# Kernel optimization log

Measured on AMD Instinct MI355X. Metric: run time of the kernel, lower is better.

The kernel has to match this reference:

```python
import jax, jax.numpy as jnp
import numpy as np
from jax import lax

STRIDES = (8, 16, 32)
REG_MAX = 16
NUM_CLASSES = 80
CLS_OUT = NUM_CLASSES + 1  # 81
REG_OUT = 4 * (REG_MAX + 1)  # 68
IN_CH = (128, 256, 512)
FEAT_HW = ((80, 80), (40, 40), (20, 20))
BATCH = 32


def _conv3(x, w, b):
    # x: [N,C,H,W], w: [O,C,3,3] -> SAME padding, stride 1
    y = lax.conv_general_dilated(x, w, (1, 1), 'SAME',
                                 dimension_numbers=('NCHW', 'OIHW', 'NCHW'))
    return y + b[None, :, None, None]


def _level_priors(h, w, stride):
    # matches get_single_level_center_priors: x fastest-varying
    xs = jnp.arange(w, dtype=jnp.float32) * stride
    ys = jnp.arange(h, dtype=jnp.float32) * stride
    x = jnp.tile(xs[None, :], (h, 1)).reshape(-1)
    y = jnp.tile(ys[:, None], (1, w)).reshape(-1)
    s = jnp.full((h * w,), float(stride), dtype=jnp.float32)
    return jnp.stack([x, y, s, s], axis=-1)  # [HW,4]


def setup_inputs() -> dict:
    key = jax.random.key(0)
    ks = jax.random.split(key, 16)
    d = {}
    for i, (c, (h, w)) in enumerate(zip(IN_CH, FEAT_HW)):
        d[f'x{i}'] = jax.random.normal(ks[i], (BATCH, c, h, w), dtype=jnp.float32)
    ki = 3
    for i, c in enumerate(IN_CH):
        d[f'wc{i}'] = jax.random.normal(ks[ki], (CLS_OUT, c, 3, 3), dtype=jnp.float32) * 0.02; ki += 1
        d[f'bc{i}'] = jnp.full((CLS_OUT,), -4.595, dtype=jnp.float32)  # bias_init_with_prob(0.01)
        d[f'wr{i}'] = jax.random.normal(ks[ki], (REG_OUT, c, 3, 3), dtype=jnp.float32) * 0.02; ki += 1
        d[f'br{i}'] = jnp.zeros((REG_OUT,), dtype=jnp.float32)
    d['scales'] = jnp.ones((3,), dtype=jnp.float32)
    return d


def reference(x0, x1, x2, wc0, bc0, wr0, br0, wc1, bc1, wr1, br1,
              wc2, bc2, wr2, br2, scales):
    xs = (x0, x1, x2)
    wcs, bcs = (wc0, wc1, wc2), (bc0, bc1, bc2)
    wrs, brs = (wr0, wr1, wr2), (br0, br1, br2)
    cls_list, box_list, prior_list = [], [], []
    for i in range(3):
        x = xs[i]
        N, _, H, W = x.shape
        # forward_single (stacked_convs=0 -> no tower convs)
        bbox = _conv3(x, wrs[i], brs[i]) * scales[i]          # [N,68,H,W]
        bbox = bbox.reshape(N, 4, REG_MAX + 1, H, W)
        bbox = jax.nn.softmax(bbox, axis=2)                   # softmax over bins
        bbox = bbox.reshape(N, 4, REG_MAX + 1, H * W).transpose(0, 3, 1, 2)  # [N,HW,4,17]
        cls = jax.nn.sigmoid(_conv3(x, wcs[i], bcs[i]))       # [N,81,H,W]
        cls = cls.reshape(N, CLS_OUT, H * W).transpose(0, 2, 1)  # [N,HW,81]
        cls_list.append(cls)
        box_list.append(bbox)
        prior_list.append(_level_priors(H, W, STRIDES[i]))
    cls_scores = jnp.concatenate(cls_list, axis=1)[:, :, :NUM_CLASSES]  # [N,A,80]
    bbox_dist = jnp.concatenate(box_list, axis=1)                        # [N,A,4,17]
    priors = jnp.concatenate(prior_list, axis=0)[None]                   # [1,A,4]
    # Integral: expectation over bins 0..reg_max
    project = jnp.arange(REG_MAX + 1, dtype=bbox_dist.dtype)
    dist = jnp.einsum('nafr,r->naf', bbox_dist, project)                 # [N,A,4]
    dist = dist * priors[..., 2, None]                                   # scale by stride
    # distance2bbox
    px, py = priors[..., 0], priors[..., 1]
    bboxes = jnp.stack([px - dist[..., 0], py - dist[..., 1],
                        px + dist[..., 2], py + dist[..., 3]], axis=-1)  # [N,A,4]
    return cls_scores, bboxes
```

## Files before the change

### kernel.cpp

```cpp
#include <hip/hip_runtime.h>
#include <hip/hip_bf16.h>
#include <math.h>

#define BATCH   32
#define A_TOTAL 8400
#define NCLS    80

typedef __attribute__((ext_vector_type(8))) short bf16x8;
typedef __attribute__((ext_vector_type(4))) float f32x4;

__device__ __forceinline__ short f2bf(float f) {
    union { float f; unsigned u; } v; v.f = f;
    unsigned u = v.u + 0x7fffu + ((v.u >> 16) & 1u);
    return (short)(u >> 16);
}

__device__ __forceinline__ void stage16(const void* g, void* ldsp) {
    __builtin_amdgcn_global_load_lds(
        (const __attribute__((address_space(1))) unsigned int*)g,
        (__attribute__((address_space(3))) unsigned int*)ldsp, 16, 0, 0);
}

template<int C>
__global__ __launch_bounds__(256) void prep_w(const float* __restrict__ wc,
                                              const float* __restrict__ wr,
                                              __hip_bfloat16* __restrict__ af) {
    const int KC = C / 32;
    const int total = 9 * KC * 10 * 64;
    int idx = blockIdx.x * 256 + threadIdx.x;
    if (idx >= total) return;
    int l   = idx & 63;
    int rem = idx >> 6;
    int mf  = rem % 10;
    int kc  = (rem / 10) % KC;
    int tap = rem / (10 * KC);
    int m     = mf * 16 + (l & 15);
    int cbase = kc * 32 + (l >> 4) * 8;
    short v[8];
#pragma unroll
    for (int j = 0; j < 8; ++j) {
        int c = cbase + j;
        float w = 0.f;
        if (m < 80)        w = wc[((size_t)m * C + c) * 9 + tap];
        else if (m < 148)  w = wr[((size_t)(m - 80) * C + c) * 9 + tap];
        v[j] = f2bf(w);
    }
    *(bf16x8*)((short*)af + (size_t)idx * 8) = *(bf16x8*)v;
}

template<int C, int H, int W>
__global__ __launch_bounds__(256) void transpose_x(const float* __restrict__ x,
                                                   __hip_bfloat16* __restrict__ xT) {
    const int CC  = C / 64;
    const int KC  = C / 32;
    const int PW  = W + 2;
    const int PHW = (H + 2) * PW;
    int b   = blockIdx.x;
    int cch = b % CC;
    int y   = (b / CC) % H;
    int n   = b / (CC * H);
    __shared__ float sm[64][W + 1];
    const float* src = x + (((size_t)n * C + cch * 64) * H + y) * W;
    for (int i = threadIdx.x; i < 64 * (W / 4); i += 256) {
        int c = i / (W / 4), f4 = i % (W / 4);
        float4 v = *(const float4*)(src + (size_t)c * H * W + f4 * 4);
        sm[c][f4 * 4 + 0] = v.x;
        sm[c][f4 * 4 + 1] = v.y;
        sm[c][f4 * 4 + 2] = v.z;
        sm[c][f4 * 4 + 3] = v.w;
    }
    __syncthreads();
    short* base = (short*)xT + (size_t)n * KC * 4 * PHW * 8;
    for (int u = threadIdx.x; u < W * 8; u += 256) {
        int g8 = u / W, xc = u % W;
        int kc = cch * 2 + (g8 >> 2);
        int j  = g8 & 3;
        short v[8];
#pragma unroll
        for (int jj = 0; jj < 8; ++jj) v[jj] = f2bf(sm[g8 * 8 + jj][xc]);
        *(bf16x8*)(base + (((size_t)(kc * 4 + j)) * PHW + (y + 1) * PW + xc + 1) * 8) =
            *(bf16x8*)v;
    }
    bf16x8 z = (bf16x8)(short)0;
    if (threadIdx.x < 16) {
        int g8 = threadIdx.x >> 1, side = threadIdx.x & 1;
        int kc = cch * 2 + (g8 >> 2), j = g8 & 3;
        *(bf16x8*)(base + (((size_t)(kc * 4 + j)) * PHW + (y + 1) * PW + side * (W + 1)) * 8) = z;
    }
    if (y == 0) {
        for (int u = threadIdx.x; u < PW * 8; u += 256) {
            int g8 = u / PW, col = u % PW;
            int kc = cch * 2 + (g8 >> 2), j = g8 & 3;
            *(bf16x8*)(base + (((size_t)(kc * 4 + j)) * PHW + col) * 8) = z;
        }
    }
    if (y == H - 1) {
        for (int u = threadIdx.x; u < PW * 8; u += 256) {
            int g8 = u / PW, col = u % PW;
            int kc = cch * 2 + (g8 >> 2), j = g8 & 3;
            *(bf16x8*)(base + (((size_t)(kc * 4 + j)) * PHW + (H + 1) * PW + col) * 8) = z;
        }
    }
}

template<int C, int H, int W, int STRIDE, int A_OFFp, int LVL, int NT, int KS, int NBLK>
__global__ __launch_bounds__(256, NBLK) void gemm_head(
    const __hip_bfloat16* __restrict__ xT,
    const __hip_bfloat16* __restrict__ af,
    const float* __restrict__ bc, const float* __restrict__ br,
    const float* __restrict__ scales,
    float* __restrict__ out_cls, float* __restrict__ out_box,
    float* __restrict__ pbuf) {
    constexpr int HW     = H * W;
    constexpr int PW     = W + 2;
    constexpr int PHW    = (H + 2) * PW;
    constexpr int NF     = NT / 32;
    constexpr int TILES  = (HW + NT - 1) / NT;
    constexpr int KC     = C / 32;
    constexpr int KCS    = KC / KS;
    constexpr int DYMAX  = (NT - 1) / W + 1;
    constexpr int NSTAGE = NT + 2 * DYMAX + 2 * W + 7;
    constexpr int NS16   = NSTAGE * 16;
    constexpr int NG     = NSTAGE * 4;
    constexpr int ITB    = (NG + 255) / 256;
    constexpr int BSZ    = ITB * 4096;
    constexpr int EPI    = 68 * (NT + 4) * 4;
    constexpr int LDSB   = (KS > 1) ? (2 * BSZ) : ((2 * BSZ) > EPI ? (2 * BSZ) : EPI);
    static_assert(ITB <= 9, "B staging spread exceeds tap steps");

    __shared__ __align__(16) char lds[LDSB];

    constexpr int NWG = BATCH * TILES * KS;
    const int bid  = blockIdx.x;
    const int swz  = (bid & 7) * (NWG / 8) + (bid >> 3);
    const int ks   = swz % KS;
    const int rest = swz / KS;
    const int tile = rest % TILES;
    const int n    = rest / TILES;

    const int tid   = threadIdx.x;
    const int l     = tid & 63;
    const int wid   = tid >> 6;
    const int mhalf = wid & 1;
    const int nhalf = wid >> 1;
    const int lr    = l & 15;
    const int kg    = l >> 4;

    const char* xb  = (const char*)xT + (size_t)n * KC * 4 * PHW * 16;
    const char* afc = (const char*)af;

    const int p0    = tile * NT;
    const int qbase = (p0 / W) * PW + (p0 % W);

    int blane[NF];
#pragma unroll
    for (int nf = 0; nf < NF; ++nf) {
        int p  = p0 + (nhalf * NF + nf) * 16 + lr;
        int qc = (p / W + 1) * PW + (p % W) + 1;
        blane[nf] = kg * NS16 + (qc - (W + 3) - qbase) * 16;
    }

    f32x4 acc[5][NF];
#pragma unroll
    for (int mf = 0; mf < 5; ++mf)
#pragma unroll
        for (int nf = 0; nf < NF; ++nf) acc[mf][nf] = (f32x4)0.f;

    auto stageB = [&](int it, int kc, unsigned dstbase) {
        int idx = it * 256 + tid;
        int j = idx / NSTAGE; if (j > 3) j = 3;
        int q = qbase + (idx - j * NSTAGE);
        if (q > PHW - 1) q = PHW - 1;
        stage16(xb + ((size_t)(kc * 4 + j) * PHW + q) * 16,
                &lds[dstbase + it * 4096 + wid * 1024]);
    };

    const int kc0 = ks * KCS;
#pragma unroll
    for (int it = 0; it < ITB; ++it) stageB(it, kc0, 0);
    __syncthreads();

    unsigned curB = 0;

#pragma unroll 1
    for (int kk = 0; kk < KCS; ++kk) {
        const int kc = kc0 + kk;
#pragma unroll
        for (int tap = 0; tap < 9; ++tap) {
            if (tap < ITB && kk + 1 < KCS)
                stageB(tap, kc + 1, curB ^ BSZ);
            const char* asrc = afc + (size_t)(tap * KC + kc) * 10240 +
                               mhalf * 5120 + l * 16;
            bf16x8 a[5];
#pragma unroll
            for (int mf = 0; mf < 5; ++mf)
                a[mf] = *(const bf16x8*)(asrc + mf * 1024);
            const int imm = ((tap / 3) * PW + (tap % 3)) * 16;
#pragma unroll
            for (int nf = 0; nf < NF; ++nf) {
                bf16x8 b = *(const bf16x8*)&lds[curB + blane[nf] + imm];
#pragma unroll
                for (int mf = 0; mf < 5; ++mf)
                    acc[mf][nf] = __builtin_amdgcn_mfma_f32_16x16x32_bf16(
                        a[mf], b, acc[mf][nf], 0, 0, 0);
            }
        }
        __syncthreads();
        curB ^= BSZ;
    }

    if constexpr (KS > 1) {
        float* pb = pbuf + (size_t)((n * TILES + tile) * KS + ks) * (160 * NT);
#pragma unroll
        for (int mf = 0; mf < 5; ++mf)
#pragma unroll
            for (int nf = 0; nf < NF; ++nf) {
                int col = (nhalf * NF + nf) * 16 + lr;
#pragma unroll
                for (int r = 0; r < 4; ++r) {
                    int ch = mhalf * 80 + mf * 16 + kg * 4 + r;
                    pb[ch * NT + col] = acc[mf][nf][r];
                }
            }
        return;
    } else {
        const float sc = scales[LVL];
        float* smf = (float*)lds;

        if (mhalf == 0) {
            float4 bias[5];
#pragma unroll
            for (int mf = 0; mf < 5; ++mf)
                bias[mf] = *(const float4*)(bc + mf * 16 + kg * 4);
#pragma unroll
            for (int nf = 0; nf < NF; ++nf) {
                int p = p0 + (nhalf * NF + nf) * 16 + lr;
                if (p < HW) {
                    float* oc = out_cls + ((size_t)n * A_TOTAL + A_OFFp + p) * NCLS;
#pragma unroll
                    for (int mf = 0; mf < 5; ++mf) {
                        f32x4 v = acc[mf][nf];
                        float4 s;
                        s.x = 1.f / (1.f + expf(-(v[0] + bias[mf].x)));
                        s.y = 1.f / (1.f + expf(-(v[1] + bias[mf].y)));
                        s.z = 1.f / (1.f + expf(-(v[2] + bias[mf].z)));
                        s.w = 1.f / (1.f + expf(-(v[3] + bias[mf].w)));
                        *(float4*)(oc + mf * 16 + kg * 4) = s;
                    }
                }
            }
        } else {
#pragma unroll
            for (int mf = 0; mf < 5; ++mf)
#pragma unroll
                for (int nf = 0; nf < NF; ++nf) {
                    int lpx = (nhalf * NF + nf) * 16 + lr;
#pragma unroll
                    for (int r = 0; r < 4; ++r) {
                        int ch = mf * 16 + kg * 4 + r;
                        if (ch < 68) smf[ch * (NT + 4) + lpx] = acc[mf][nf][r];
                    }
                }
        }
        __syncthreads();

#pragma unroll
        for (int uu = 0; uu < NT / 64; ++uu) {
            int u   = uu * 256 + tid;
            int f   = u >> 7;
            int lpx = u & 127;
            if (NT == 64) { f = (u >> 6) & 3; lpx = u & 63; }
            int p = p0 + lpx;
            if (f < 4 && p < HW) {
                float lg[17];
                float m = -1e30f;
#pragma unroll
                for (int r = 0; r < 17; ++r) {
                    lg[r] = (smf[(f * 17 + r) * (NT + 4) + lpx] + br[f * 17 + r]) * sc;
                    m = fmaxf(m, lg[r]);
                }
                float ssum = 0.f, esum = 0.f;
#pragma unroll
                for (int r = 0; r < 17; ++r) {
                    float e = expf(lg[r] - m);
                    ssum += e;
                    esum += e * (float)r;
                }
                const float dist = esum / ssum * (float)STRIDE;
                const int py = p / W, px = p % W;
                const float base = (f & 1) ? (float)(py * STRIDE) : (float)(px * STRIDE);
                const float val  = (f < 2) ? (base - dist) : (base + dist);
                out_box[((size_t)n * A_TOTAL + A_OFFp + p) * 4 + f] = val;
            }
        }
    }
}

template<int H, int W, int STRIDE, int A_OFFp, int LVL, int TILES, int KS>
__global__ __launch_bounds__(256) void reduce_epi(
    const float* __restrict__ pbuf,
    const float* __restrict__ bc, const float* __restrict__ br,
    const float* __restrict__ scales,
    float* __restrict__ out_cls, float* __restrict__ out_box) {
    constexpr int HW = H * W;
    const int bid  = blockIdx.x;
    const int tile = bid % TILES;
    const int n    = bid / TILES;
    const int tid  = threadIdx.x;
    const float* pb = pbuf + (size_t)(n * TILES + tile) * KS * 10240;

    __shared__ float smf[160 * 66];
    for (int idx = tid; idx < 160 * 64; idx += 256) {
        float s = 0.f;
#pragma unroll
        for (int k = 0; k < KS; ++k) s += pb[k * 10240 + idx];
        smf[(idx >> 6) * 66 + (idx & 63)] = s;
    }
    __syncthreads();

    const int q = tid >> 6;
    const int t = tid & 63;
    const int p = tile * 64 + t;
    if (p < HW) {
        float* oc = out_cls + ((size_t)n * A_TOTAL + A_OFFp + p) * NCLS + q * 20;
#pragma unroll
        for (int k = 0; k < 20; k += 4) {
            float4 v;
            v.x = 1.f / (1.f + expf(-(smf[(q * 20 + k + 0) * 66 + t] + bc[q * 20 + k + 0])));
            v.y = 1.f / (1.f + expf(-(smf[(q * 20 + k + 1) * 66 + t] + bc[q * 20 + k + 1])));
            v.z = 1.f / (1.f + expf(-(smf[(q * 20 + k + 2) * 66 + t] + bc[q * 20 + k + 2])));
            v.w = 1.f / (1.f + expf(-(smf[(q * 20 + k + 3) * 66 + t] + bc[q * 20 + k + 3])));
            *(float4*)(oc + k) = v;
        }
        const float sc = scales[LVL];
        float lg[17];
        float m = -1e30f;
#pragma unroll
        for (int r = 0; r < 17; ++r) {
            lg[r] = (smf[(80 + q * 17 + r) * 66 + t] + br[q * 17 + r]) * sc;
            m = fmaxf(m, lg[r]);
        }
        float ssum = 0.f, esum = 0.f;
#pragma unroll
        for (int r = 0; r < 17; ++r) {
            float e = expf(lg[r] - m);
            ssum += e;
            esum += e * (float)r;
        }
        const float dist = esum / ssum * (float)STRIDE;
        const int py = p / W, px = p % W;
        const float base = (q & 1) ? (float)(py * STRIDE) : (float)(px * STRIDE);
        const float val  = (q < 2) ? (base - dist) : (base + dist);
        out_box[((size_t)n * A_TOTAL + A_OFFp + p) * 4 + q] = val;
    }
}

extern "C" void kernel_launch(void* const* d_in, const int* in_sizes, int n_in,
                              void* d_out, int out_size, void* d_ws, size_t ws_size,
                              hipStream_t stream) {
    const float* x0  = (const float*)d_in[0];
    const float* x1  = (const float*)d_in[1];
    const float* x2  = (const float*)d_in[2];
    const float* wc0 = (const float*)d_in[3];
    const float* bc0 = (const float*)d_in[4];
    const float* wr0 = (const float*)d_in[5];
    const float* br0 = (const float*)d_in[6];
    const float* wc1 = (const float*)d_in[7];
    const float* bc1 = (const float*)d_in[8];
    const float* wr1 = (const float*)d_in[9];
    const float* br1 = (const float*)d_in[10];
    const float* wc2 = (const float*)d_in[11];
    const float* bc2 = (const float*)d_in[12];
    const float* wr2 = (const float*)d_in[13];
    const float* br2 = (const float*)d_in[14];
    const float* scl = (const float*)d_in[15];

    float* out_cls = (float*)d_out;
    float* out_box = (float*)d_out + (size_t)BATCH * A_TOTAL * NCLS;

    __hip_bfloat16* af  = (__hip_bfloat16*)d_ws;
    __hip_bfloat16* af0 = af;
    __hip_bfloat16* af1 = af + 184320;
    __hip_bfloat16* af2 = af + 552960;
    __hip_bfloat16* xT  = af + 1290240;
    float* pbuf = (float*)((char*)xT + 15859712);

    prep_w<128><<<dim3(90),  256, 0, stream>>>(wc0, wr0, af0);
    prep_w<256><<<dim3(180), 256, 0, stream>>>(wc1, wr1, af1);
    prep_w<512><<<dim3(360), 256, 0, stream>>>(wc2, wr2, af2);

    transpose_x<128, 80, 80><<<dim3(32 * 80 * 2), 256, 0, stream>>>(x0, xT);
    gemm_head<128, 80, 80, 8, 0, 0, 128, 1, 3><<<dim3(32 * 50), 256, 0, stream>>>(
        xT, af0, bc0, br0, scl, out_cls, out_box, nullptr);

    transpose_x<256, 40, 40><<<dim3(32 * 40 * 4), 256, 0, stream>>>(x1, xT);
    gemm_head<256, 40, 40, 16, 6400, 1, 64, 1, 4><<<dim3(32 * 25), 256, 0, stream>>>(
        xT, af1, bc1, br1, scl, out_cls, out_box, nullptr);

    transpose_x<512, 20, 20><<<dim3(32 * 20 * 8), 256, 0, stream>>>(x2, xT);
    gemm_head<512, 20, 20, 32, 8000, 2, 64, 4, 4><<<dim3(32 * 7 * 4), 256, 0, stream>>>(
        xT, af2, bc2, br2, scl, out_cls, out_box, pbuf);
    reduce_epi<20, 20, 32, 8000, 2, 7, 4><<<dim3(32 * 7), 256, 0, stream>>>(
        pbuf, bc2, br2, scl, out_cls, out_box);
}
```

Before: 281.2 us.

## Prefetch A fragments one tap ahead, use fast sigmoid/exp, retune level tiles

The GEMM inner loop now loads the weight (A) fragments for the next tap into a second register set while the current tap's MFMAs run, hiding global load latency. Sigmoid and softmax switch to __expf and hardware reciprocal, and the box epilogue loop is generalised to any tile width. The level-1 launch moves to 96-pixel tiles with fewer blocks, and the last template parameter changes for levels 1 and 2. The changes cost extra VGPRs and slightly lower-precision transcendentals, and the prefetch on the final step reads one A block past the end.

```diff
diff --git a/kernel.cpp b/kernel.cpp
--- a/kernel.cpp
+++ b/kernel.cpp
@@ -13,6 +13,10 @@
     union { float f; unsigned u; } v; v.f = f;
     unsigned u = v.u + 0x7fffu + ((v.u >> 16) & 1u);
     return (short)(u >> 16);
+}
+
+__device__ __forceinline__ float fsig(float x) {
+    return __builtin_amdgcn_rcpf(1.f + __expf(-x));
 }
 
 __device__ __forceinline__ void stage16(const void* g, void* ldsp) {
@@ -174,8 +178,18 @@
         stage16(xb + ((size_t)(kc * 4 + j) * PHW + q) * 16,
                 &lds[dstbase + it * 4096 + wid * 1024]);
     };
+    auto loadA = [&](bf16x8* dst, int step) {
+        const char* asrc = afc + (size_t)step * 10240 + mhalf * 5120 + l * 16;
+#pragma unroll
+        for (int mf = 0; mf < 5; ++mf)
+            dst[mf] = *(const bf16x8*)(asrc + mf * 1024);
+    };
 
     const int kc0 = ks * KCS;
+
+    bf16x8 acur[5], anxt[5];
+    loadA(acur, kc0);
+
 #pragma unroll
     for (int it = 0; it < ITB; ++it) stageB(it, kc0, 0);
     __syncthreads();
@@ -189,12 +203,8 @@
         for (int tap = 0; tap < 9; ++tap) {
             if (tap < ITB && kk + 1 < KCS)
                 stageB(tap, kc + 1, curB ^ BSZ);
-            const char* asrc = afc + (size_t)(tap * KC + kc) * 10240 +
-                               mhalf * 5120 + l * 16;
-            bf16x8 a[5];
-#pragma unroll
-            for (int mf = 0; mf < 5; ++mf)
-                a[mf] = *(const bf16x8*)(asrc + mf * 1024);
+            const int nstep = (tap == 8) ? (kc + 1) : ((tap + 1) * KC + kc);
+            loadA(anxt, nstep);
             const int imm = ((tap / 3) * PW + (tap % 3)) * 16;
 #pragma unroll
             for (int nf = 0; nf < NF; ++nf) {
@@ -202,8 +212,10 @@
 #pragma unroll
                 for (int mf = 0; mf < 5; ++mf)
                     acc[mf][nf] = __builtin_amdgcn_mfma_f32_16x16x32_bf16(
-                        a[mf], b, acc[mf][nf], 0, 0, 0);
+                        acur[mf], b, acc[mf][nf], 0, 0, 0);
             }
+#pragma unroll
+            for (int mf = 0; mf < 5; ++mf) acur[mf] = anxt[mf];
         }
         __syncthreads();
         curB ^= BSZ;
@@ -241,10 +253,10 @@
                     for (int mf = 0; mf < 5; ++mf) {
                         f32x4 v = acc[mf][nf];
                         float4 s;
-                        s.x = 1.f / (1.f + expf(-(v[0] + bias[mf].x)));
-                        s.y = 1.f / (1.f + expf(-(v[1] + bias[mf].y)));
-                        s.z = 1.f / (1.f + expf(-(v[2] + bias[mf].z)));
-                        s.w = 1.f / (1.f + expf(-(v[3] + bias[mf].w)));
+                        s.x = fsig(v[0] + bias[mf].x);
+                        s.y = fsig(v[1] + bias[mf].y);
+                        s.z = fsig(v[2] + bias[mf].z);
+                        s.w = fsig(v[3] + bias[mf].w);
                         *(float4*)(oc + mf * 16 + kg * 4) = s;
                     }
                 }
@@ -264,14 +276,11 @@
         }
         __syncthreads();
 
-#pragma unroll
-        for (int uu = 0; uu < NT / 64; ++uu) {
-            int u   = uu * 256 + tid;
-            int f   = u >> 7;
-            int lpx = u & 127;
-            if (NT == 64) { f = (u >> 6) & 3; lpx = u & 63; }
-            int p = p0 + lpx;
-            if (f < 4 && p < HW) {
+        for (int u = tid; u < 4 * NT; u += 256) {
+            int f   = u / NT;
+            int lpx = u % NT;
+            int p   = p0 + lpx;
+            if (p < HW) {
                 float lg[17];
                 float m = -1e30f;
 #pragma unroll
@@ -282,11 +291,11 @@
                 float ssum = 0.f, esum = 0.f;
 #pragma unroll
                 for (int r = 0; r < 17; ++r) {
-                    float e = expf(lg[r] - m);
+                    float e = __expf(lg[r] - m);
                     ssum += e;
                     esum += e * (float)r;
                 }
-                const float dist = esum / ssum * (float)STRIDE;
+                const float dist = esum * __builtin_amdgcn_rcpf(ssum) * (float)STRIDE;
                 const int py = p / W, px = p % W;
                 const float base = (f & 1) ? (float)(py * STRIDE) : (float)(px * STRIDE);
                 const float val  = (f < 2) ? (base - dist) : (base + dist);
@@ -326,10 +335,10 @@
 #pragma unroll
         for (int k = 0; k < 20; k += 4) {
             float4 v;
-            v.x = 1.f / (1.f + expf(-(smf[(q * 20 + k + 0) * 66 + t] + bc[q * 20 + k + 0])));
-            v.y = 1.f / (1.f + expf(-(smf[(q * 20 + k + 1) * 66 + t] + bc[q * 20 + k + 1])));
-            v.z = 1.f / (1.f + expf(-(smf[(q * 20 + k + 2) * 66 + t] + bc[q * 20 + k + 2])));
-            v.w = 1.f / (1.f + expf(-(smf[(q * 20 + k + 3) * 66 + t] + bc[q * 20 + k + 3])));
+            v.x = fsig(smf[(q * 20 + k + 0) * 66 + t] + bc[q * 20 + k + 0]);
+            v.y = fsig(smf[(q * 20 + k + 1) * 66 + t] + bc[q * 20 + k + 1]);
+            v.z = fsig(smf[(q * 20 + k + 2) * 66 + t] + bc[q * 20 + k + 2]);
+            v.w = fsig(smf[(q * 20 + k + 3) * 66 + t] + bc[q * 20 + k + 3]);
             *(float4*)(oc + k) = v;
         }
         const float sc = scales[LVL];
@@ -343,11 +352,11 @@
         float ssum = 0.f, esum = 0.f;
 #pragma unroll
         for (int r = 0; r < 17; ++r) {
-            float e = expf(lg[r] - m);
+            float e = __expf(lg[r] - m);
             ssum += e;
             esum += e * (float)r;
         }
-        const float dist = esum / ssum * (float)STRIDE;
+        const float dist = esum * __builtin_amdgcn_rcpf(ssum) * (float)STRIDE;
         const int py = p / W, px = p % W;
         const float base = (q & 1) ? (float)(py * STRIDE) : (float)(px * STRIDE);
         const float val  = (q < 2) ? (base - dist) : (base + dist);
@@ -394,11 +403,11 @@
         xT, af0, bc0, br0, scl, out_cls, out_box, nullptr);
 
     transpose_x<256, 40, 40><<<dim3(32 * 40 * 4), 256, 0, stream>>>(x1, xT);
-    gemm_head<256, 40, 40, 16, 6400, 1, 64, 1, 4><<<dim3(32 * 25), 256, 0, stream>>>(
+    gemm_head<256, 40, 40, 16, 6400, 1, 96, 1, 3><<<dim3(32 * 17), 256, 0, stream>>>(
         xT, af1, bc1, br1, scl, out_cls, out_box, nullptr);
 
     transpose_x<512, 20, 20><<<dim3(32 * 20 * 8), 256, 0, stream>>>(x2, xT);
-    gemm_head<512, 20, 20, 32, 8000, 2, 64, 4, 4><<<dim3(32 * 7 * 4), 256, 0, stream>>>(
+    gemm_head<512, 20, 20, 32, 8000, 2, 64, 4, 3><<<dim3(32 * 7 * 4), 256, 0, stream>>>(
         xT, af2, bc2, br2, scl, out_cls, out_box, pbuf);
     reduce_epi<20, 20, 32, 8000, 2, 7, 4><<<dim3(32 * 7), 256, 0, stream>>>(
         pbuf, bc2, br2, scl, out_cls, out_box);
```

New measurement: 258.4 us. -8.1%, faster.
